# Optimization experiments

Hardware: AMD Instinct MI355X
Metric: run time of the kernel (lower is better)

The kernel has to match this reference:

```python
import jax, jax.numpy as jnp
import numpy as np

B, T, D = 1, 4096, 2048
NUM_HEADS, NUM_KV_HEADS, HEAD_DIM = 16, 8, 128
QUERY_PRE_ATTN_SCALAR = HEAD_DIM ** -0.5
SOFT_CAP = 50.0
WINDOW = 1024
ROPE_BASE = 10000.0
ROPE_SCALE = 1.0
K_MASK = -2.3819763e+38


def apply_rope(x, positions, head_dim, max_wavelength=ROPE_BASE, scale_factor=ROPE_SCALE):
    # x: [B, T, N, H], positions: [B, T]
    fraction = 2.0 * jnp.arange(head_dim // 2, dtype=jnp.float32) / head_dim
    timescale = max_wavelength ** fraction  # [H/2]
    sinusoid = positions[..., None].astype(jnp.float32) / timescale  # [B, T, H/2]
    sinusoid = (sinusoid / scale_factor)[..., None, :]  # [B, T, 1, H/2]
    sin, cos = jnp.sin(sinusoid), jnp.cos(sinusoid)
    first, second = jnp.split(x, 2, axis=-1)
    out = jnp.concatenate([first * cos - second * sin,
                           second * cos + first * sin], axis=-1)
    return out.astype(x.dtype)


def setup_inputs() -> dict:
    key = jax.random.key(0)
    ks = jax.random.split(key, 4)
    x = jax.random.normal(ks[0], (B, T, D), dtype=jnp.float32)
    segment_pos = jnp.broadcast_to(jnp.arange(T, dtype=jnp.int32), (B, T))
    # causal mask [B, T, S]
    attn_mask = jnp.broadcast_to(
        jnp.tril(jnp.ones((T, T), dtype=jnp.bool_)), (B, T, T))
    q_w = jax.random.normal(ks[1], (NUM_HEADS, D, HEAD_DIM), dtype=jnp.float32) * 0.02
    kv_w = jax.random.normal(ks[2], (2, NUM_KV_HEADS, D, HEAD_DIM), dtype=jnp.float32) * 0.02
    o_w = jax.random.normal(ks[3], (NUM_HEADS, HEAD_DIM, D), dtype=jnp.float32) * 0.02
    return {"x": x, "segment_pos": segment_pos, "attn_mask": attn_mask,
            "q_w": q_w, "kv_w": kv_w, "o_w": o_w}


def reference(x, segment_pos, attn_mask, q_w, kv_w, o_w):
    # Projections (GQA: separate q and kv einsums)
    q = jnp.einsum('BTD,NDH->BTNH', x, q_w)          # [B,T,N,H]
    k = jnp.einsum('BSD,KDH->BSKH', x, kv_w[0])      # [B,S,K,H]
    v = jnp.einsum('BSD,KDH->BSKH', x, kv_w[1])      # [B,S,K,H]

    q = apply_rope(q, segment_pos, HEAD_DIM)
    q = q * QUERY_PRE_ATTN_SCALAR
    k = apply_rope(k, segment_pos, HEAD_DIM)

    num_groups = NUM_HEADS // NUM_KV_HEADS
    qg = q.reshape(B, T, NUM_KV_HEADS, num_groups, HEAD_DIM)
    logits = jnp.einsum('BTKGH,BSKH->BTKGS', qg, k)
    logits = logits.reshape(B, T, NUM_HEADS, -1)     # [B,T,N,S]

    # soft cap
    logits = jnp.tanh(logits / SOFT_CAP) * SOFT_CAP

    # sliding-window mask combined with causal mask
    all_ones = jnp.ones_like(attn_mask)
    sliding = jnp.triu(all_ones, -WINDOW + 1) * jnp.tril(all_ones, WINDOW - 1)
    mask = sliding * attn_mask                       # [B,T,S] bool

    padded = jnp.where(mask[:, :, None, :], logits, K_MASK)
    probs = jax.nn.softmax(padded, axis=-1).astype(k.dtype)

    probs_g = probs.reshape(B, T, NUM_KV_HEADS, num_groups, -1)
    encoded = jnp.einsum('BTKGS,BSKH->BTKGH', probs_g, v)
    encoded = encoded.reshape(B, T, NUM_HEADS, HEAD_DIM)

    attn_output = jnp.einsum('BTNH,NHD->BTD', encoded, o_w)
    return attn_output
```

## Files before the change

kernel.cpp:

```cpp
#include <hip/hip_runtime.h>
#include <hip/hip_bf16.h>
#include <math.h>

typedef __attribute__((ext_vector_type(8))) short short8;
typedef __attribute__((ext_vector_type(8))) unsigned short ushort8;
typedef __attribute__((ext_vector_type(4))) float f32x4;
typedef __attribute__((ext_vector_type(2))) float f32x2;

#define T_SEQ 4096
#define D_MODEL 2048
#define N_HEADS 16
#define N_KV 8
#define HEAD_DIM 128
#define QSCALE 0.08838834764831845f

__device__ __forceinline__ float bf2f(unsigned short u) {
  union { unsigned int i; float f; } x; x.i = ((unsigned int)u) << 16; return x.f;
}
__device__ __forceinline__ unsigned short f2bf(float f) {
  union { float f; unsigned int i; } x; x.f = f;
  unsigned int i = x.i;
  unsigned int r = i + 0x7fffu + ((i >> 16) & 1u);
  return (unsigned short)(r >> 16);
}

__global__ __launch_bounds__(256) void prep_kernel(const float* __restrict__ x,
                                                   unsigned short* __restrict__ xb,
                                                   const int* __restrict__ segpos,
                                                   float2* __restrict__ tab) {
  int b = blockIdx.x;
  if (b < 4096) {
    int idx = b * 256 + threadIdx.x;
    const float4* p = reinterpret_cast<const float4*>(x) + (size_t)idx * 2;
    float4 a = p[0], c = p[1];
    ushort8 o;
    o[0] = f2bf(a.x); o[1] = f2bf(a.y); o[2] = f2bf(a.z); o[3] = f2bf(a.w);
    o[4] = f2bf(c.x); o[5] = f2bf(c.y); o[6] = f2bf(c.z); o[7] = f2bf(c.w);
    reinterpret_cast<ushort8*>(xb)[idx] = o;
  } else {
    int idx = (b - 4096) * 256 + threadIdx.x;
    int t = idx >> 6, i = idx & 63;
    float pos = (float)segpos[t];
    float ts = powf(10000.f, (float)(2 * i) / 128.f);
    float ang = pos / ts;
    tab[idx] = make_float2(sinf(ang), cosf(ang));
  }
}

__global__ __launch_bounds__(256) void wqkv_transpose_kernel(const float* __restrict__ q_w,
                                                             const float* __restrict__ kv_w,
                                                             unsigned short* __restrict__ Wt) {
  __shared__ float tile[32][33];
  int z = blockIdx.z;
  const float* src = (z < 16) ? q_w + (size_t)z * 2048 * 128
                              : kv_w + (size_t)(z - 16) * 2048 * 128;
  unsigned short* dst = Wt + (size_t)z * 128 * 2048;
  int c0 = blockIdx.x * 32, r0 = blockIdx.y * 32;
  int tx = threadIdx.x & 31, ty = threadIdx.x >> 5;
#pragma unroll
  for (int i = 0; i < 4; ++i)
    tile[ty + i * 8][tx] = src[(size_t)(r0 + ty + i * 8) * 128 + c0 + tx];
  __syncthreads();
#pragma unroll
  for (int i = 0; i < 4; ++i)
    dst[(size_t)(c0 + ty + i * 8) * 2048 + r0 + tx] = f2bf(tile[tx][ty + i * 8]);
}

__global__ __launch_bounds__(256) void ow_transpose_kernel(const float* __restrict__ src,
                                                           unsigned short* __restrict__ dst) {
  __shared__ float tile[32][33];
  int c0 = blockIdx.x * 32, r0 = blockIdx.y * 32;
  int tx = threadIdx.x & 31, ty = threadIdx.x >> 5;
#pragma unroll
  for (int i = 0; i < 4; ++i)
    tile[ty + i * 8][tx] = src[(size_t)(r0 + ty + i * 8) * 2048 + c0 + tx];
  __syncthreads();
#pragma unroll
  for (int i = 0; i < 4; ++i)
    dst[(size_t)(c0 + ty + i * 8) * 2048 + r0 + tx] = f2bf(tile[tx][ty + i * 8]);
}

#define G2L(gp, lp)                                                           \
  __builtin_amdgcn_global_load_lds(                                           \
      (const __attribute__((address_space(1))) void*)(gp),                    \
      (__attribute__((address_space(3))) void*)(lp), 16, 0, 0)
#define GBAR() asm volatile("s_barrier" ::: "memory")
#define VMW(n) asm volatile("s_waitcnt vmcnt(" #n ")" ::: "memory")
#define LG0()  asm volatile("s_waitcnt lgkmcnt(0)" ::: "memory")

template <int OUT_BF16, int MHB>
__global__ __launch_bounds__(512, 2) void gemm256_kernel(const unsigned short* __restrict__ A,
                                                         const unsigned short* __restrict__ Bt,
                                                         void* __restrict__ Cout,
                                                         int M, int N, int K) {
  extern __shared__ unsigned short smem[];
  unsigned short* ldsA = smem;
  unsigned short* ldsB = smem + 2 * MHB * 8192;
  const int tid = threadIdx.x;
  const int lane = tid & 63, wave = tid >> 6;
  const int wm = wave >> 2, wn = wave & 3;
  const int lr = lane & 15, lg = lane >> 4;
  const int swz = (lr & 7) << 3;
  const int c0s = (lg * 8) ^ swz;
  const int c1s = (32 + lg * 8) ^ swz;

  int id = blockIdx.y * gridDim.x + blockIdx.x;
  int nb = gridDim.x * gridDim.y;
  int sw = (id & 7) * (nb >> 3) + (id >> 3);
  const long brow = (long)(sw / gridDim.x) * (128 * MHB);
  const long bcol = (long)(sw % gridDim.x) * 256;

  const unsigned short* Ag = A + brow * K;
  const unsigned short* Bg = Bt + bcol * K;

  const int r0 = tid >> 3;
  const int cs = ((tid & 7) * 8) ^ ((r0 & 7) << 3);

#define ST_A(tt, b, a)                                                        \
  { G2L(Ag + (size_t)((a) * 128 + r0) * K + (size_t)(tt) * 64 + cs,           \
        ldsA + (b) * (MHB * 8192) + (a) * 8192 + tid * 8);                    \
    G2L(Ag + (size_t)((a) * 128 + r0 + 64) * K + (size_t)(tt) * 64 + cs,      \
        ldsA + (b) * (MHB * 8192) + (a) * 8192 + 4096 + tid * 8); }
#define ST_B(tt, b, h)                                                        \
  { G2L(Bg + (size_t)((h) * 128 + r0) * K + (size_t)(tt) * 64 + cs,           \
        ldsB + (b) * 16384 + (h) * 8192 + tid * 8);                           \
    G2L(Bg + (size_t)((h) * 128 + r0 + 64) * K + (size_t)(tt) * 64 + cs,      \
        ldsB + (b) * 16384 + (h) * 8192 + 4096 + tid * 8); }

  f32x4 acc[4 * MHB][4] = {};
  short8 bf[4][2];
  short8 af[4];

#define RD_B(b)                                                               \
  { const unsigned short* pb = ldsB + (b) * 16384 + wn * 4096;                \
    _Pragma("unroll")                                                         \
    for (int n = 0; n < 4; ++n) {                                             \
      bf[n][0] = *(const short8*)(pb + (n * 16 + lr) * 64 + c0s);             \
      bf[n][1] = *(const short8*)(pb + (n * 16 + lr) * 64 + c1s);             \
    } }
#define RD_A(b, mb)                                                           \
  { const unsigned short* pa = ldsA + (b) * (MHB * 8192) + wm * (MHB * 4096); \
    af[0] = *(const short8*)(pa + ((mb) * 16 + lr) * 64 + c0s);               \
    af[1] = *(const short8*)(pa + ((mb) * 16 + lr) * 64 + c1s);               \
    af[2] = *(const short8*)(pa + ((mb) * 16 + 16 + lr) * 64 + c0s);          \
    af[3] = *(const short8*)(pa + ((mb) * 16 + 16 + lr) * 64 + c1s); }
#define MFMA2(mb)                                                             \
  { __builtin_amdgcn_s_setprio(1);                                            \
    _Pragma("unroll")                                                         \
    for (int n = 0; n < 4; ++n) {                                             \
      acc[mb][n]     = __builtin_amdgcn_mfma_f32_16x16x32_bf16(af[0], bf[n][0], acc[mb][n], 0, 0, 0);     \
      acc[mb][n]     = __builtin_amdgcn_mfma_f32_16x16x32_bf16(af[1], bf[n][1], acc[mb][n], 0, 0, 0);     \
      acc[mb + 1][n] = __builtin_amdgcn_mfma_f32_16x16x32_bf16(af[2], bf[n][0], acc[mb + 1][n], 0, 0, 0); \
      acc[mb + 1][n] = __builtin_amdgcn_mfma_f32_16x16x32_bf16(af[3], bf[n][1], acc[mb + 1][n], 0, 0, 0); \
    }                                                                         \
    __builtin_amdgcn_s_setprio(0); }

  const int NT = K >> 6;

  if constexpr (MHB == 2) {
    ST_B(0, 0, 0); ST_B(0, 0, 1); ST_A(0, 0, 0); ST_A(0, 0, 1);
    ST_B(1, 1, 0); ST_B(1, 1, 1);
    VMW(4); GBAR();
    for (int j = 0; j < (NT >> 1); ++j) {
      const int c1 = 2 * j + 1, t2 = 2 * j + 2, t3 = 2 * j + 3;
      const bool s2 = t2 < NT, s3 = t3 < NT;
      RD_B(0); RD_A(0, 0); ST_A(c1, 1, 0);
      GBAR(); LG0(); MFMA2(0); GBAR();
      RD_A(0, 2); ST_A(c1, 1, 1);
      if (s2) ST_B(t2, 0, 0);
      GBAR(); LG0(); MFMA2(2); GBAR();
      RD_A(0, 4);
      if (s2) ST_B(t2, 0, 1);
      GBAR(); LG0(); MFMA2(4); GBAR();
      RD_A(0, 6);
      if (s2) { VMW(4); } else { VMW(0); }
      GBAR(); LG0(); MFMA2(6); GBAR();
      RD_B(1); RD_A(1, 0);
      if (s2) ST_A(t2, 0, 0);
      GBAR(); LG0(); MFMA2(0); GBAR();
      RD_A(1, 2);
      if (s2) ST_A(t2, 0, 1);
      if (s3) ST_B(t3, 1, 0);
      GBAR(); LG0(); MFMA2(2); GBAR();
      RD_A(1, 4);
      if (s3) ST_B(t3, 1, 1);
      GBAR(); LG0(); MFMA2(4); GBAR();
      RD_A(1, 6);
      if (s3) { VMW(4); } else { VMW(0); }
      GBAR(); LG0(); MFMA2(6); GBAR();
    }
  } else {
    ST_B(0, 0, 0); ST_B(0, 0, 1); ST_A(0, 0, 0);
    ST_B(1, 1, 0); ST_B(1, 1, 1);
    VMW(4); GBAR();
    for (int j = 0; j < (NT >> 1); ++j) {
      const int c1 = 2 * j + 1, t2 = 2 * j + 2, t3 = 2 * j + 3;
      const bool s2 = t2 < NT, s3 = t3 < NT;
      RD_B(0); RD_A(0, 0); ST_A(c1, 1, 0);
      GBAR(); LG0(); MFMA2(0); GBAR();
      RD_A(0, 2);
      if (s2) { ST_B(t2, 0, 0); ST_B(t2, 0, 1); VMW(4); } else { VMW(0); }
      GBAR(); LG0(); MFMA2(2); GBAR();
      RD_B(1); RD_A(1, 0);
      if (s2) ST_A(t2, 0, 0);
      GBAR(); LG0(); MFMA2(0); GBAR();
      RD_A(1, 2);
      if (s3) { ST_B(t3, 1, 0); ST_B(t3, 1, 1); VMW(4); } else { VMW(0); }
      GBAR(); LG0(); MFMA2(2); GBAR();
    }
  }

#undef ST_A
#undef ST_B
#undef RD_A
#undef RD_B
#undef MFMA2

#pragma unroll
  for (int m = 0; m < 4 * MHB; ++m) {
#pragma unroll
    for (int i = 0; i < 4; ++i) {
      long row = brow + wm * (64 * MHB) + m * 16 + lg * 4 + i;
#pragma unroll
      for (int n = 0; n < 4; ++n) {
        long col = bcol + wn * 64 + n * 16 + lr;
        if (OUT_BF16)
          ((unsigned short*)Cout)[row * N + col] = f2bf(acc[m][n][i]);
        else
          ((float*)Cout)[row * N + col] = acc[m][n][i];
      }
    }
  }
}

__global__ __launch_bounds__(256) void rope_vt_kernel(const unsigned short* __restrict__ raw,
                                                      const float2* __restrict__ tab,
                                                      unsigned short* __restrict__ Qb,
                                                      unsigned short* __restrict__ Kb,
                                                      unsigned short* __restrict__ Vt) {
  __shared__ unsigned short tile[32][33];
  int b = blockIdx.x;
  if (b < 3072) {
    int gid = b * 256 + threadIdx.x;
    int j = gid & 7;
    int rem = gid >> 3;
    int hs = rem % 24;
    int t = rem / 24;
    int i0 = j * 8;
    float sv[8], cv[8];
    const float2* tp = tab + t * 64 + i0;
#pragma unroll
    for (int q = 0; q < 8; ++q) { float2 sc2 = tp[q]; sv[q] = sc2.x; cv[q] = sc2.y; }
    if (hs < 16) {
      const unsigned short* p = raw + (size_t)t * 4096 + hs * 128 + i0;
      ushort8 a = *(const ushort8*)p;
      ushort8 c = *(const ushort8*)(p + 64);
      ushort8 o1, o2;
#pragma unroll
      for (int q = 0; q < 8; ++q) {
        float fa = bf2f(a[q]), fb = bf2f(c[q]);
        o1[q] = f2bf((fa * cv[q] - fb * sv[q]) * QSCALE);
        o2[q] = f2bf((fb * cv[q] + fa * sv[q]) * QSCALE);
      }
      unsigned short* qp = Qb + ((size_t)hs * T_SEQ + t) * 128 + i0;
      *(ushort8*)qp = o1;
      *(ushort8*)(qp + 64) = o2;
    } else {
      int kn = hs - 16;
      const unsigned short* p = raw + (size_t)t * 4096 + 2048 + kn * 128 + i0;
      ushort8 a = *(const ushort8*)p;
      ushort8 c = *(const ushort8*)(p + 64);
      ushort8 o1, o2;
#pragma unroll
      for (int q = 0; q < 8; ++q) {
        float fa = bf2f(a[q]), fb = bf2f(c[q]);
        o1[q] = f2bf(fa * cv[q] - fb * sv[q]);
        o2[q] = f2bf(fb * cv[q] + fa * sv[q]);
      }
      unsigned short* kp = Kb + ((size_t)kn * T_SEQ + t) * 128 + i0;
      *(ushort8*)kp = o1;
      *(ushort8*)(kp + 64) = o2;
    }
  } else {
    int id = b - 3072;
    int bx = id & 3, by = (id >> 2) & 127, bz = id >> 9;
    const unsigned short* src = raw + 3072 + (size_t)bz * 128;
    unsigned short* dst = Vt + (size_t)bz * 128 * 4096;
    int c0 = bx * 32, r0 = by * 32;
    int tx = threadIdx.x & 31, ty = threadIdx.x >> 5;
#pragma unroll
    for (int i = 0; i < 4; ++i)
      tile[ty + i * 8][tx] = src[(size_t)(r0 + ty + i * 8) * 4096 + c0 + tx];
    __syncthreads();
#pragma unroll
    for (int i = 0; i < 4; ++i)
      dst[(size_t)(c0 + ty + i * 8) * 4096 + r0 + tx] = tile[tx][ty + i * 8];
  }
}

__global__ __launch_bounds__(512, 2) void attn_kernel(const unsigned short* __restrict__ Qb,
                                                      const unsigned short* __restrict__ Kb,
                                                      const unsigned short* __restrict__ Vt,
                                                      unsigned short* __restrict__ enc) {
  __shared__ unsigned short Ks[2][64][128];
  __shared__ unsigned short Vs[2][128][64];
  __shared__ unsigned short Ps[8][32][72];
  int rawb = blockIdx.x;
  int lin = (rawb & 7) * 32 + (rawb >> 3);
  const int h = lin >> 4;
  const int qb0 = (lin & 15) * 256;
  const int kvh = h >> 1;
  const int tid = threadIdx.x, lane = tid & 63, wave = tid >> 6;
  const int qw = qb0 + wave * 32;
  const int lr = lane & 15, lg = lane >> 4;
  const int sw = (lr & 7) << 3;
  const int ck0 = (lg * 8) ^ sw, ck1 = (32 + lg * 8) ^ sw;
  const int ck2 = (64 + lg * 8) ^ sw, ck3 = (96 + lg * 8) ^ sw;

  short8 aq[2][4];
#pragma unroll
  for (int g = 0; g < 2; ++g) {
    const unsigned short* qp = Qb + ((size_t)h * T_SEQ + qw + g * 16 + lr) * 128 + lg * 8;
#pragma unroll
    for (int c = 0; c < 4; ++c) aq[g][c] = *(const short8*)(qp + c * 32);
  }
  f32x4 acc[2][8] = {};
  float lsum[2] = {0.f, 0.f};

  const int s_lo = (qb0 - 1023) > 0 ? (qb0 - 1023) : 0;
  const int kb_lo = s_lo >> 6, kb_hi = (qb0 + 255) >> 6;

  const int rK = tid >> 4;
  const int cpK = (tid & 15) * 8;
  const int colK = cpK ^ ((rK & 7) << 3);
  const int rV = tid >> 3;
  const int cpV = (tid & 7) * 8;
  const int colV = cpV ^ ((rV & 7) << 3);
  const unsigned short* kgb = Kb + ((size_t)kvh * T_SEQ + rK) * 128 + colK;
  const unsigned short* vgb = Vt + ((size_t)kvh * 128 + rV) * T_SEQ + colV;

  ushort8 kr0, kr1, vr0, vr1;
  {
    const int s0g = kb_lo * 64;
    kr0 = *(const ushort8*)(kgb + (size_t)s0g * 128);
    kr1 = *(const ushort8*)(kgb + (size_t)(s0g + 32) * 128);
    vr0 = *(const ushort8*)(vgb + s0g);
    vr1 = *(const ushort8*)(vgb + (size_t)64 * T_SEQ + s0g);
  }

  const int qg0 = qw + lr, qg1 = qw + 16 + lr;
  for (int kb = kb_lo; kb <= kb_hi; ++kb) {
    const int s0g = kb * 64;
    const int buf = kb & 1;
    *(ushort8*)&Ks[buf][rK][cpK] = kr0;
    *(ushort8*)&Ks[buf][rK + 32][cpK] = kr1;
    *(ushort8*)&Vs[buf][rV][cpV] = vr0;
    *(ushort8*)&Vs[buf][rV + 64][cpV] = vr1;
    __syncthreads();
    if (kb < kb_hi) {
      const int sn = s0g + 64;
      kr0 = *(const ushort8*)(kgb + (size_t)sn * 128);
      kr1 = *(const ushort8*)(kgb + (size_t)(sn + 32) * 128);
      vr0 = *(const ushort8*)(vgb + sn);
      vr1 = *(const ushort8*)(vgb + (size_t)64 * T_SEQ + sn);
    }
    if (s0g > qw + 31 || s0g + 63 < qw - 1023) continue;
    const bool interior = (s0g + 63 <= qw) && (s0g >= qw - 992);

    f32x4 sT0[4] = {}, sT1[4] = {};
    __builtin_amdgcn_s_setprio(1);
#pragma unroll
    for (int st = 0; st < 4; ++st) {
      const unsigned short* kp = &Ks[buf][st * 16 + lr][0];
      short8 k0 = *(const short8*)(kp + ck0);
      short8 k1 = *(const short8*)(kp + ck1);
      short8 k2 = *(const short8*)(kp + ck2);
      short8 k3 = *(const short8*)(kp + ck3);
      sT0[st] = __builtin_amdgcn_mfma_f32_16x16x32_bf16(k0, aq[0][0], sT0[st], 0, 0, 0);
      sT1[st] = __builtin_amdgcn_mfma_f32_16x16x32_bf16(k0, aq[1][0], sT1[st], 0, 0, 0);
      sT0[st] = __builtin_amdgcn_mfma_f32_16x16x32_bf16(k1, aq[0][1], sT0[st], 0, 0, 0);
      sT1[st] = __builtin_amdgcn_mfma_f32_16x16x32_bf16(k1, aq[1][1], sT1[st], 0, 0, 0);
      sT0[st] = __builtin_amdgcn_mfma_f32_16x16x32_bf16(k2, aq[0][2], sT0[st], 0, 0, 0);
      sT1[st] = __builtin_amdgcn_mfma_f32_16x16x32_bf16(k2, aq[1][2], sT1[st], 0, 0, 0);
      sT0[st] = __builtin_amdgcn_mfma_f32_16x16x32_bf16(k3, aq[0][3], sT0[st], 0, 0, 0);
      sT1[st] = __builtin_amdgcn_mfma_f32_16x16x32_bf16(k3, aq[1][3], sT1[st], 0, 0, 0);
    }
    __builtin_amdgcn_s_setprio(0);

#pragma unroll
    for (int g = 0; g < 2; ++g) {
      const f32x4* sTg = g ? sT1 : sT0;
      const int qgg = g ? qg1 : qg0;
#pragma unroll
      for (int st = 0; st < 4; ++st) {
        f32x4 svv = sTg[st];
        f32x2 sa, sb;
        sa[0] = svv[0]; sa[1] = svv[1]; sb[0] = svv[2]; sb[1] = svv[3];
        f32x2 ua = sa * sa, ub = sb * sb;
        f32x2 numa = ua * 4.0e-4f + 15.f, numb = ub * 4.0e-4f + 15.f;
        f32x2 dena = ua * 2.4e-3f + 15.f, denb = ub * 2.4e-3f + 15.f;
        f32x2 ra, rb;
        ra[0] = __builtin_amdgcn_rcpf(dena[0]); ra[1] = __builtin_amdgcn_rcpf(dena[1]);
        rb[0] = __builtin_amdgcn_rcpf(denb[0]); rb[1] = __builtin_amdgcn_rcpf(denb[1]);
        f32x2 ea = (sa * 1.44269504f) * numa * ra;
        f32x2 eb = (sb * 1.44269504f) * numb * rb;
        float e[4] = {ea[0], ea[1], eb[0], eb[1]};
        float p[4];
#pragma unroll
        for (int r = 0; r < 4; ++r) {
          if (!interior) {
            int sg = s0g + st * 16 + lg * 4 + r;
            e[r] = ((unsigned)(qgg - sg) <= 1023u) ? e[r] : -__builtin_inff();
          }
          asm("v_exp_f32 %0, %1" : "=v"(p[r]) : "v"(e[r]));
        }
        lsum[g] += (p[0] + p[1]) + (p[2] + p[3]);
        unsigned u0, u1;
        asm("v_cvt_pk_bf16_f32 %0, %1, %2" : "=v"(u0) : "v"(p[0]), "v"(p[1]));
        asm("v_cvt_pk_bf16_f32 %0, %1, %2" : "=v"(u1) : "v"(p[2]), "v"(p[3]));
        uint2 w; w.x = u0; w.y = u1;
        *(uint2*)&Ps[wave][g * 16 + lr][st * 16 + lg * 4] = w;
      }
    }
    short8 pa00 = *(const short8*)&Ps[wave][lr][lg * 8];
    short8 pa01 = *(const short8*)&Ps[wave][lr][32 + lg * 8];
    short8 pa10 = *(const short8*)&Ps[wave][16 + lr][lg * 8];
    short8 pa11 = *(const short8*)&Ps[wave][16 + lr][32 + lg * 8];
    __builtin_amdgcn_s_setprio(1);
#pragma unroll
    for (int d0 = 0; d0 < 8; ++d0) {
      const unsigned short* vp = &Vs[buf][d0 * 16 + lr][0];
      short8 bv0 = *(const short8*)(vp + ((lg * 8) ^ sw));
      short8 bv1 = *(const short8*)(vp + ((32 + lg * 8) ^ sw));
      acc[0][d0] = __builtin_amdgcn_mfma_f32_16x16x32_bf16(pa00, bv0, acc[0][d0], 0, 0, 0);
      acc[1][d0] = __builtin_amdgcn_mfma_f32_16x16x32_bf16(pa10, bv0, acc[1][d0], 0, 0, 0);
      acc[0][d0] = __builtin_amdgcn_mfma_f32_16x16x32_bf16(pa01, bv1, acc[0][d0], 0, 0, 0);
      acc[1][d0] = __builtin_amdgcn_mfma_f32_16x16x32_bf16(pa11, bv1, acc[1][d0], 0, 0, 0);
    }
    __builtin_amdgcn_s_setprio(0);
  }

#pragma unroll
  for (int g = 0; g < 2; ++g) {
    float l = lsum[g];
    l += __shfl_xor(l, 16);
    l += __shfl_xor(l, 32);
#pragma unroll
    for (int r = 0; r < 4; ++r) {
      float lt = __shfl(l, lg * 4 + r);
      float inv = __builtin_amdgcn_rcpf(lt);
      int row = qw + g * 16 + lg * 4 + r;
      unsigned short* op = enc + (size_t)row * D_MODEL + h * 128 + lr;
#pragma unroll
      for (int d0 = 0; d0 < 8; ++d0) op[d0 * 16] = f2bf(acc[g][d0][r] * inv);
    }
  }
}

extern "C" void kernel_launch(void* const* d_in, const int* in_sizes, int n_in,
                              void* d_out, int out_size, void* d_ws, size_t ws_size,
                              hipStream_t stream) {
  const float* x = (const float*)d_in[0];
  const int* segpos = (const int*)d_in[1];
  const float* q_w = (const float*)d_in[3];
  const float* kv_w = (const float*)d_in[4];
  const float* o_w = (const float*)d_in[5];
  float* out = (float*)d_out;
  char* ws = (char*)d_ws;

  const size_t OFF_XB = 0;
  const size_t OFF_WT = OFF_XB + 16777216;
  const size_t OFF_RAW = OFF_WT + 16777216;
  const size_t OFF_KB = OFF_RAW + 33554432;
  const size_t OFF_VT = OFF_KB + 8388608;
  const size_t OFF_TAB = OFF_VT + 8388608;
  unsigned short* xb = (unsigned short*)(ws + OFF_XB);
  unsigned short* Wt = (unsigned short*)(ws + OFF_WT);
  unsigned short* raw = (unsigned short*)(ws + OFF_RAW);
  unsigned short* Kb = (unsigned short*)(ws + OFF_KB);
  unsigned short* Vt = (unsigned short*)(ws + OFF_VT);
  float2* tab = (float2*)(ws + OFF_TAB);
  unsigned short* o_wt = xb;
  unsigned short* Qb = Wt;
  unsigned short* enc = raw;

  hipFuncSetAttribute((const void*)(gemm256_kernel<1, 2>),
                      hipFuncAttributeMaxDynamicSharedMemorySize, 131072);
  hipFuncSetAttribute((const void*)(gemm256_kernel<0, 1>),
                      hipFuncAttributeMaxDynamicSharedMemorySize, 98304);

  prep_kernel<<<dim3(5120), dim3(256), 0, stream>>>(x, xb, segpos, tab);
  wqkv_transpose_kernel<<<dim3(4, 64, 32), dim3(256), 0, stream>>>(q_w, kv_w, Wt);
  gemm256_kernel<1, 2><<<dim3(16, 16), dim3(512), 131072, stream>>>(xb, Wt, (void*)raw, 4096, 4096, 2048);
  ow_transpose_kernel<<<dim3(64, 64), dim3(256), 0, stream>>>(o_w, o_wt);
  rope_vt_kernel<<<dim3(7168), dim3(256), 0, stream>>>(raw, tab, Qb, Kb, Vt);
  attn_kernel<<<dim3(256), dim3(512), 0, stream>>>(Qb, Kb, Vt, enc);
  gemm256_kernel<0, 1><<<dim3(8, 32), dim3(512), 98304, stream>>>(enc, o_wt, (void*)out, 4096, 2048, 2048);
}
```

Baseline: 197.4 us.

## Use triple-buffered LDS pipeline for the output-projection GEMM

Adds a dedicated GEMM kernel for the output projection (128x256 tiles) that uses a three-stage LDS ring buffer, prefetching two K-tiles ahead instead of one. The QKV GEMM template drops its MHB parameter and keeps only the 256x256 path. The aim is to hide more global-load latency in the out-projection GEMM. In exchange it uses 144 KB of LDS per block, limiting occupancy to one block per CU.

```diff
diff --git a/kernel.cpp b/kernel.cpp
--- a/kernel.cpp
+++ b/kernel.cpp
@@ -88,14 +88,14 @@
 #define VMW(n) asm volatile("s_waitcnt vmcnt(" #n ")" ::: "memory")
 #define LG0()  asm volatile("s_waitcnt lgkmcnt(0)" ::: "memory")
 
-template <int OUT_BF16, int MHB>
+template <int OUT_BF16>
 __global__ __launch_bounds__(512, 2) void gemm256_kernel(const unsigned short* __restrict__ A,
                                                          const unsigned short* __restrict__ Bt,
                                                          void* __restrict__ Cout,
                                                          int M, int N, int K) {
   extern __shared__ unsigned short smem[];
   unsigned short* ldsA = smem;
-  unsigned short* ldsB = smem + 2 * MHB * 8192;
+  unsigned short* ldsB = smem + 32768;
   const int tid = threadIdx.x;
   const int lane = tid & 63, wave = tid >> 6;
   const int wm = wave >> 2, wn = wave & 3;
@@ -107,7 +107,7 @@
   int id = blockIdx.y * gridDim.x + blockIdx.x;
   int nb = gridDim.x * gridDim.y;
   int sw = (id & 7) * (nb >> 3) + (id >> 3);
-  const long brow = (long)(sw / gridDim.x) * (128 * MHB);
+  const long brow = (long)(sw / gridDim.x) * 256;
   const long bcol = (long)(sw % gridDim.x) * 256;
 
   const unsigned short* Ag = A + brow * K;
@@ -118,16 +118,16 @@
 
 #define ST_A(tt, b, a)                                                        \
   { G2L(Ag + (size_t)((a) * 128 + r0) * K + (size_t)(tt) * 64 + cs,           \
-        ldsA + (b) * (MHB * 8192) + (a) * 8192 + tid * 8);                    \
+        ldsA + (b) * 16384 + (a) * 8192 + tid * 8);                           \
     G2L(Ag + (size_t)((a) * 128 + r0 + 64) * K + (size_t)(tt) * 64 + cs,      \
-        ldsA + (b) * (MHB * 8192) + (a) * 8192 + 4096 + tid * 8); }
+        ldsA + (b) * 16384 + (a) * 8192 + 4096 + tid * 8); }
 #define ST_B(tt, b, h)                                                        \
   { G2L(Bg + (size_t)((h) * 128 + r0) * K + (size_t)(tt) * 64 + cs,           \
         ldsB + (b) * 16384 + (h) * 8192 + tid * 8);                           \
     G2L(Bg + (size_t)((h) * 128 + r0 + 64) * K + (size_t)(tt) * 64 + cs,      \
         ldsB + (b) * 16384 + (h) * 8192 + 4096 + tid * 8); }
 
-  f32x4 acc[4 * MHB][4] = {};
+  f32x4 acc[8][4] = {};
   short8 bf[4][2];
   short8 af[4];
 
@@ -139,7 +139,7 @@
       bf[n][1] = *(const short8*)(pb + (n * 16 + lr) * 64 + c1s);             \
     } }
 #define RD_A(b, mb)                                                           \
-  { const unsigned short* pa = ldsA + (b) * (MHB * 8192) + wm * (MHB * 4096); \
+  { const unsigned short* pa = ldsA + (b) * 16384 + wm * 8192;                \
     af[0] = *(const short8*)(pa + ((mb) * 16 + lr) * 64 + c0s);               \
     af[1] = *(const short8*)(pa + ((mb) * 16 + lr) * 64 + c1s);               \
     af[2] = *(const short8*)(pa + ((mb) * 16 + 16 + lr) * 64 + c0s);          \
@@ -156,71 +156,43 @@
     __builtin_amdgcn_s_setprio(0); }
 
   const int NT = K >> 6;
-
-  if constexpr (MHB == 2) {
-    ST_B(0, 0, 0); ST_B(0, 0, 1); ST_A(0, 0, 0); ST_A(0, 0, 1);
-    ST_B(1, 1, 0); ST_B(1, 1, 1);
-    VMW(4); GBAR();
-    for (int j = 0; j < (NT >> 1); ++j) {
-      const int c1 = 2 * j + 1, t2 = 2 * j + 2, t3 = 2 * j + 3;
-      const bool s2 = t2 < NT, s3 = t3 < NT;
-      RD_B(0); RD_A(0, 0); ST_A(c1, 1, 0);
-      GBAR(); LG0(); MFMA2(0); GBAR();
-      RD_A(0, 2); ST_A(c1, 1, 1);
-      if (s2) ST_B(t2, 0, 0);
-      GBAR(); LG0(); MFMA2(2); GBAR();
-      RD_A(0, 4);
-      if (s2) ST_B(t2, 0, 1);
-      GBAR(); LG0(); MFMA2(4); GBAR();
-      RD_A(0, 6);
-      if (s2) { VMW(4); } else { VMW(0); }
-      GBAR(); LG0(); MFMA2(6); GBAR();
-      RD_B(1); RD_A(1, 0);
-      if (s2) ST_A(t2, 0, 0);
-      GBAR(); LG0(); MFMA2(0); GBAR();
-      RD_A(1, 2);
-      if (s2) ST_A(t2, 0, 1);
-      if (s3) ST_B(t3, 1, 0);
-      GBAR(); LG0(); MFMA2(2); GBAR();
-      RD_A(1, 4);
-      if (s3) ST_B(t3, 1, 1);
-      GBAR(); LG0(); MFMA2(4); GBAR();
-      RD_A(1, 6);
-      if (s3) { VMW(4); } else { VMW(0); }
-      GBAR(); LG0(); MFMA2(6); GBAR();
-    }
-  } else {
-    ST_B(0, 0, 0); ST_B(0, 0, 1); ST_A(0, 0, 0);
-    ST_B(1, 1, 0); ST_B(1, 1, 1);
-    VMW(4); GBAR();
-    for (int j = 0; j < (NT >> 1); ++j) {
-      const int c1 = 2 * j + 1, t2 = 2 * j + 2, t3 = 2 * j + 3;
-      const bool s2 = t2 < NT, s3 = t3 < NT;
-      RD_B(0); RD_A(0, 0); ST_A(c1, 1, 0);
-      GBAR(); LG0(); MFMA2(0); GBAR();
-      RD_A(0, 2);
-      if (s2) { ST_B(t2, 0, 0); ST_B(t2, 0, 1); VMW(4); } else { VMW(0); }
-      GBAR(); LG0(); MFMA2(2); GBAR();
-      RD_B(1); RD_A(1, 0);
-      if (s2) ST_A(t2, 0, 0);
-      GBAR(); LG0(); MFMA2(0); GBAR();
-      RD_A(1, 2);
-      if (s3) { ST_B(t3, 1, 0); ST_B(t3, 1, 1); VMW(4); } else { VMW(0); }
-      GBAR(); LG0(); MFMA2(2); GBAR();
-    }
-  }
-
-#undef ST_A
-#undef ST_B
-#undef RD_A
-#undef RD_B
-#undef MFMA2
-
-#pragma unroll
-  for (int m = 0; m < 4 * MHB; ++m) {
+  ST_B(0, 0, 0); ST_B(0, 0, 1); ST_A(0, 0, 0); ST_A(0, 0, 1);
+  ST_B(1, 1, 0); ST_B(1, 1, 1);
+  VMW(4); GBAR();
+  for (int j = 0; j < (NT >> 1); ++j) {
+    const int c1 = 2 * j + 1, t2 = 2 * j + 2, t3 = 2 * j + 3;
+    const bool s2 = t2 < NT, s3 = t3 < NT;
+    RD_B(0); RD_A(0, 0); ST_A(c1, 1, 0);
+    GBAR(); LG0(); MFMA2(0); GBAR();
+    RD_A(0, 2); ST_A(c1, 1, 1);
+    if (s2) ST_B(t2, 0, 0);
+    GBAR(); LG0(); MFMA2(2); GBAR();
+    RD_A(0, 4);
+    if (s2) ST_B(t2, 0, 1);
+    GBAR(); LG0(); MFMA2(4); GBAR();
+    RD_A(0, 6);
+    if (s2) { VMW(4); } else { VMW(0); }
+    GBAR(); LG0(); MFMA2(6); GBAR();
+    RD_B(1); RD_A(1, 0);
+    if (s2) ST_A(t2, 0, 0);
+    GBAR(); LG0(); MFMA2(0); GBAR();
+    RD_A(1, 2);
+    if (s2) ST_A(t2, 0, 1);
+    if (s3) ST_B(t3, 1, 0);
+    GBAR(); LG0(); MFMA2(2); GBAR();
+    RD_A(1, 4);
+    if (s3) ST_B(t3, 1, 1);
+    GBAR(); LG0(); MFMA2(4); GBAR();
+    RD_A(1, 6);
+    if (s3) { VMW(4); } else { VMW(0); }
+    GBAR(); LG0(); MFMA2(6); GBAR();
+  }
+
+#pragma unroll
+  for (int m = 0; m < 8; ++m) {
 #pragma unroll
     for (int i = 0; i < 4; ++i) {
-      long row = brow + wm * (64 * MHB) + m * 16 + lg * 4 + i;
+      long row = brow + wm * 128 + m * 16 + lg * 4 + i;
 #pragma unroll
       for (int n = 0; n < 4; ++n) {
         long col = bcol + wn * 64 + n * 16 + lr;
@@ -231,6 +203,113 @@
       }
     }
   }
+#undef ST_A
+#undef ST_B
+#undef RD_A
+#undef RD_B
+#undef MFMA2
+}
+
+__global__ __launch_bounds__(512, 1) void gemm_op3_kernel(const unsigned short* __restrict__ A,
+                                                          const unsigned short* __restrict__ Bt,
+                                                          float* __restrict__ Cout,
+                                                          int M, int N, int K) {
+  extern __shared__ unsigned short smem[];
+  unsigned short* ldsA = smem;
+  unsigned short* ldsB = smem + 3 * 8192;
+  const int tid = threadIdx.x;
+  const int lane = tid & 63, wave = tid >> 6;
+  const int wm = wave >> 2, wn = wave & 3;
+  const int lr = lane & 15, lg = lane >> 4;
+  const int swz = (lr & 7) << 3;
+  const int c0s = (lg * 8) ^ swz;
+  const int c1s = (32 + lg * 8) ^ swz;
+
+  int id = blockIdx.y * gridDim.x + blockIdx.x;
+  int nb = gridDim.x * gridDim.y;
+  int sw = (id & 7) * (nb >> 3) + (id >> 3);
+  const long brow = (long)(sw / gridDim.x) * 128;
+  const long bcol = (long)(sw % gridDim.x) * 256;
+
+  const unsigned short* Ag = A + brow * K;
+  const unsigned short* Bg = Bt + bcol * K;
+
+  const int r0 = tid >> 3;
+  const int cs = ((tid & 7) * 8) ^ ((r0 & 7) << 3);
+
+#define ST_A3(tt, b)                                                          \
+  { G2L(Ag + (size_t)(r0) * K + (size_t)(tt) * 64 + cs,                       \
+        ldsA + (b) * 8192 + tid * 8);                                         \
+    G2L(Ag + (size_t)(r0 + 64) * K + (size_t)(tt) * 64 + cs,                  \
+        ldsA + (b) * 8192 + 4096 + tid * 8); }
+#define ST_B3(tt, b, h)                                                       \
+  { G2L(Bg + (size_t)((h) * 128 + r0) * K + (size_t)(tt) * 64 + cs,           \
+        ldsB + (b) * 16384 + (h) * 8192 + tid * 8);                           \
+    G2L(Bg + (size_t)((h) * 128 + r0 + 64) * K + (size_t)(tt) * 64 + cs,      \
+        ldsB + (b) * 16384 + (h) * 8192 + 4096 + tid * 8); }
+
+  f32x4 acc[4][4] = {};
+  short8 bf[4][2];
+  short8 af[4];
+
+#define RD_B3(b)                                                              \
+  { const unsigned short* pb = ldsB + (b) * 16384 + wn * 4096;                \
+    _Pragma("unroll")                                                         \
+    for (int n = 0; n < 4; ++n) {                                             \
+      bf[n][0] = *(const short8*)(pb + (n * 16 + lr) * 64 + c0s);             \
+      bf[n][1] = *(const short8*)(pb + (n * 16 + lr) * 64 + c1s);             \
+    } }
+#define RD_A3(b, mb)                                                          \
+  { const unsigned short* pa = ldsA + (b) * 8192 + wm * 4096;                 \
+    af[0] = *(const short8*)(pa + ((mb) * 16 + lr) * 64 + c0s);               \
+    af[1] = *(const short8*)(pa + ((mb) * 16 + lr) * 64 + c1s);               \
+    af[2] = *(const short8*)(pa + ((mb) * 16 + 16 + lr) * 64 + c0s);          \
+    af[3] = *(const short8*)(pa + ((mb) * 16 + 16 + lr) * 64 + c1s); }
+#define MFMA2(mb)                                                             \
+  { __builtin_amdgcn_s_setprio(1);                                            \
+    _Pragma("unroll")                                                         \
+    for (int n = 0; n < 4; ++n) {                                             \
+      acc[mb][n]     = __builtin_amdgcn_mfma_f32_16x16x32_bf16(af[0], bf[n][0], acc[mb][n], 0, 0, 0);     \
+      acc[mb][n]     = __builtin_amdgcn_mfma_f32_16x16x32_bf16(af[1], bf[n][1], acc[mb][n], 0, 0, 0);     \
+      acc[mb + 1][n] = __builtin_amdgcn_mfma_f32_16x16x32_bf16(af[2], bf[n][0], acc[mb + 1][n], 0, 0, 0); \
+      acc[mb + 1][n] = __builtin_amdgcn_mfma_f32_16x16x32_bf16(af[3], bf[n][1], acc[mb + 1][n], 0, 0, 0); \
+    }                                                                         \
+    __builtin_amdgcn_s_setprio(0); }
+
+  const int NT = K >> 6;
+  ST_B3(0, 0, 0); ST_B3(0, 0, 1); ST_A3(0, 0);
+  ST_B3(1, 1, 0); ST_B3(1, 1, 1); ST_A3(1, 1);
+  VMW(6); GBAR();
+  int b = 0;
+  for (int t = 0; t < NT; ++t) {
+    int bn = b + 2; if (bn >= 3) bn -= 3;
+    const bool st = (t + 2) < NT;
+    RD_B3(b); RD_A3(b, 0);
+    if (st) { ST_B3(t + 2, bn, 0); ST_B3(t + 2, bn, 1); }
+    GBAR(); LG0(); MFMA2(0); GBAR();
+    RD_A3(b, 2);
+    if (st) { ST_A3(t + 2, bn); VMW(6); } else { VMW(0); }
+    GBAR(); LG0(); MFMA2(2); GBAR();
+    b = b + 1; if (b >= 3) b = 0;
+  }
+
+#pragma unroll
+  for (int m = 0; m < 4; ++m) {
+#pragma unroll
+    for (int i = 0; i < 4; ++i) {
+      long row = brow + wm * 64 + m * 16 + lg * 4 + i;
+#pragma unroll
+      for (int n = 0; n < 4; ++n) {
+        long col = bcol + wn * 64 + n * 16 + lr;
+        Cout[row * N + col] = acc[m][n][i];
+      }
+    }
+  }
+#undef ST_A3
+#undef ST_B3
+#undef RD_A3
+#undef RD_B3
+#undef MFMA2
 }
 
 __global__ __launch_bounds__(256) void rope_vt_kernel(const unsigned short* __restrict__ raw,
@@ -484,16 +563,16 @@
   unsigned short* Qb = Wt;
   unsigned short* enc = raw;
 
-  hipFuncSetAttribute((const void*)(gemm256_kernel<1, 2>),
+  hipFuncSetAttribute((const void*)(gemm256_kernel<1>),
                       hipFuncAttributeMaxDynamicSharedMemorySize, 131072);
-  hipFuncSetAttribute((const void*)(gemm256_kernel<0, 1>),
-                      hipFuncAttributeMaxDynamicSharedMemorySize, 98304);
+  hipFuncSetAttribute((const void*)gemm_op3_kernel,
+                      hipFuncAttributeMaxDynamicSharedMemorySize, 147456);
 
   prep_kernel<<<dim3(5120), dim3(256), 0, stream>>>(x, xb, segpos, tab);
   wqkv_transpose_kernel<<<dim3(4, 64, 32), dim3(256), 0, stream>>>(q_w, kv_w, Wt);
-  gemm256_kernel<1, 2><<<dim3(16, 16), dim3(512), 131072, stream>>>(xb, Wt, (void*)raw, 4096, 4096, 2048);
+  gemm256_kernel<1><<<dim3(16, 16), dim3(512), 131072, stream>>>(xb, Wt, (void*)raw, 4096, 4096, 2048);
   ow_transpose_kernel<<<dim3(64, 64), dim3(256), 0, stream>>>(o_w, o_wt);
   rope_vt_kernel<<<dim3(7168), dim3(256), 0, stream>>>(raw, tab, Qb, Kb, Vt);
   attn_kernel<<<dim3(256), dim3(512), 0, stream>>>(Qb, Kb, Vt, enc);
-  gemm256_kernel<0, 1><<<dim3(8, 32), dim3(512), 98304, stream>>>(enc, o_wt, (void*)out, 4096, 2048, 2048);
-}
+  gemm_op3_kernel<<<dim3(8, 32), dim3(512), 147456, stream>>>(enc, o_wt, out, 4096, 2048, 2048);
+}
```

Measured after the change: 199.1 us. Within noise of the previous version (+0.9%).

## Split-K output projection with atomics and fuse o_w transpose into rope kernel

Applied to the files above, without the earlier changes.

The output-projection GEMM now uses 256x256 tiles with a split-K of 2 over the grid z dimension, accumulating into a zeroed fp32 output with atomic adds. The o_w transpose is folded into the rope/V-transpose kernel as extra blocks, which removes one launch. The GEMM template is unified around the 2-row-half schedule. The extra cost is a memset of the output and atomic traffic to global memory, and the float summation order becomes nondeterministic.

```diff
diff --git a/kernel.cpp b/kernel.cpp
--- a/kernel.cpp
+++ b/kernel.cpp
@@ -66,20 +66,6 @@
     dst[(size_t)(c0 + ty + i * 8) * 2048 + r0 + tx] = f2bf(tile[tx][ty + i * 8]);
 }
 
-__global__ __launch_bounds__(256) void ow_transpose_kernel(const float* __restrict__ src,
-                                                           unsigned short* __restrict__ dst) {
-  __shared__ float tile[32][33];
-  int c0 = blockIdx.x * 32, r0 = blockIdx.y * 32;
-  int tx = threadIdx.x & 31, ty = threadIdx.x >> 5;
-#pragma unroll
-  for (int i = 0; i < 4; ++i)
-    tile[ty + i * 8][tx] = src[(size_t)(r0 + ty + i * 8) * 2048 + c0 + tx];
-  __syncthreads();
-#pragma unroll
-  for (int i = 0; i < 4; ++i)
-    dst[(size_t)(c0 + ty + i * 8) * 2048 + r0 + tx] = f2bf(tile[tx][ty + i * 8]);
-}
-
 #define G2L(gp, lp)                                                           \
   __builtin_amdgcn_global_load_lds(                                           \
       (const __attribute__((address_space(1))) void*)(gp),                    \
@@ -88,14 +74,14 @@
 #define VMW(n) asm volatile("s_waitcnt vmcnt(" #n ")" ::: "memory")
 #define LG0()  asm volatile("s_waitcnt lgkmcnt(0)" ::: "memory")
 
-template <int OUT_BF16, int MHB>
+template <int OUT_MODE>
 __global__ __launch_bounds__(512, 2) void gemm256_kernel(const unsigned short* __restrict__ A,
                                                          const unsigned short* __restrict__ Bt,
                                                          void* __restrict__ Cout,
                                                          int M, int N, int K) {
   extern __shared__ unsigned short smem[];
   unsigned short* ldsA = smem;
-  unsigned short* ldsB = smem + 2 * MHB * 8192;
+  unsigned short* ldsB = smem + 32768;
   const int tid = threadIdx.x;
   const int lane = tid & 63, wave = tid >> 6;
   const int wm = wave >> 2, wn = wave & 3;
@@ -107,27 +93,30 @@
   int id = blockIdx.y * gridDim.x + blockIdx.x;
   int nb = gridDim.x * gridDim.y;
   int sw = (id & 7) * (nb >> 3) + (id >> 3);
-  const long brow = (long)(sw / gridDim.x) * (128 * MHB);
+  const long brow = (long)(sw / gridDim.x) * 256;
   const long bcol = (long)(sw % gridDim.x) * 256;
-
-  const unsigned short* Ag = A + brow * K;
-  const unsigned short* Bg = Bt + bcol * K;
+  long koff = 0;
+  int klen = K;
+  if constexpr (OUT_MODE == 2) { klen = K >> 1; koff = (long)blockIdx.z * klen; }
+
+  const unsigned short* Ag = A + brow * K + koff;
+  const unsigned short* Bg = Bt + bcol * K + koff;
 
   const int r0 = tid >> 3;
   const int cs = ((tid & 7) * 8) ^ ((r0 & 7) << 3);
 
 #define ST_A(tt, b, a)                                                        \
   { G2L(Ag + (size_t)((a) * 128 + r0) * K + (size_t)(tt) * 64 + cs,           \
-        ldsA + (b) * (MHB * 8192) + (a) * 8192 + tid * 8);                    \
+        ldsA + (b) * 16384 + (a) * 8192 + tid * 8);                           \
     G2L(Ag + (size_t)((a) * 128 + r0 + 64) * K + (size_t)(tt) * 64 + cs,      \
-        ldsA + (b) * (MHB * 8192) + (a) * 8192 + 4096 + tid * 8); }
+        ldsA + (b) * 16384 + (a) * 8192 + 4096 + tid * 8); }
 #define ST_B(tt, b, h)                                                        \
   { G2L(Bg + (size_t)((h) * 128 + r0) * K + (size_t)(tt) * 64 + cs,           \
         ldsB + (b) * 16384 + (h) * 8192 + tid * 8);                           \
     G2L(Bg + (size_t)((h) * 128 + r0 + 64) * K + (size_t)(tt) * 64 + cs,      \
         ldsB + (b) * 16384 + (h) * 8192 + 4096 + tid * 8); }
 
-  f32x4 acc[4 * MHB][4] = {};
+  f32x4 acc[8][4] = {};
   short8 bf[4][2];
   short8 af[4];
 
@@ -139,7 +128,7 @@
       bf[n][1] = *(const short8*)(pb + (n * 16 + lr) * 64 + c1s);             \
     } }
 #define RD_A(b, mb)                                                           \
-  { const unsigned short* pa = ldsA + (b) * (MHB * 8192) + wm * (MHB * 4096); \
+  { const unsigned short* pa = ldsA + (b) * 16384 + wm * 8192;                \
     af[0] = *(const short8*)(pa + ((mb) * 16 + lr) * 64 + c0s);               \
     af[1] = *(const short8*)(pa + ((mb) * 16 + lr) * 64 + c1s);               \
     af[2] = *(const short8*)(pa + ((mb) * 16 + 16 + lr) * 64 + c0s);          \
@@ -155,90 +144,70 @@
     }                                                                         \
     __builtin_amdgcn_s_setprio(0); }
 
-  const int NT = K >> 6;
-
-  if constexpr (MHB == 2) {
-    ST_B(0, 0, 0); ST_B(0, 0, 1); ST_A(0, 0, 0); ST_A(0, 0, 1);
-    ST_B(1, 1, 0); ST_B(1, 1, 1);
-    VMW(4); GBAR();
-    for (int j = 0; j < (NT >> 1); ++j) {
-      const int c1 = 2 * j + 1, t2 = 2 * j + 2, t3 = 2 * j + 3;
-      const bool s2 = t2 < NT, s3 = t3 < NT;
-      RD_B(0); RD_A(0, 0); ST_A(c1, 1, 0);
-      GBAR(); LG0(); MFMA2(0); GBAR();
-      RD_A(0, 2); ST_A(c1, 1, 1);
-      if (s2) ST_B(t2, 0, 0);
-      GBAR(); LG0(); MFMA2(2); GBAR();
-      RD_A(0, 4);
-      if (s2) ST_B(t2, 0, 1);
-      GBAR(); LG0(); MFMA2(4); GBAR();
-      RD_A(0, 6);
-      if (s2) { VMW(4); } else { VMW(0); }
-      GBAR(); LG0(); MFMA2(6); GBAR();
-      RD_B(1); RD_A(1, 0);
-      if (s2) ST_A(t2, 0, 0);
-      GBAR(); LG0(); MFMA2(0); GBAR();
-      RD_A(1, 2);
-      if (s2) ST_A(t2, 0, 1);
-      if (s3) ST_B(t3, 1, 0);
-      GBAR(); LG0(); MFMA2(2); GBAR();
-      RD_A(1, 4);
-      if (s3) ST_B(t3, 1, 1);
-      GBAR(); LG0(); MFMA2(4); GBAR();
-      RD_A(1, 6);
-      if (s3) { VMW(4); } else { VMW(0); }
-      GBAR(); LG0(); MFMA2(6); GBAR();
-    }
-  } else {
-    ST_B(0, 0, 0); ST_B(0, 0, 1); ST_A(0, 0, 0);
-    ST_B(1, 1, 0); ST_B(1, 1, 1);
-    VMW(4); GBAR();
-    for (int j = 0; j < (NT >> 1); ++j) {
-      const int c1 = 2 * j + 1, t2 = 2 * j + 2, t3 = 2 * j + 3;
-      const bool s2 = t2 < NT, s3 = t3 < NT;
-      RD_B(0); RD_A(0, 0); ST_A(c1, 1, 0);
-      GBAR(); LG0(); MFMA2(0); GBAR();
-      RD_A(0, 2);
-      if (s2) { ST_B(t2, 0, 0); ST_B(t2, 0, 1); VMW(4); } else { VMW(0); }
-      GBAR(); LG0(); MFMA2(2); GBAR();
-      RD_B(1); RD_A(1, 0);
-      if (s2) ST_A(t2, 0, 0);
-      GBAR(); LG0(); MFMA2(0); GBAR();
-      RD_A(1, 2);
-      if (s3) { ST_B(t3, 1, 0); ST_B(t3, 1, 1); VMW(4); } else { VMW(0); }
-      GBAR(); LG0(); MFMA2(2); GBAR();
-    }
-  }
-
+  const int NT = klen >> 6;
+  ST_B(0, 0, 0); ST_B(0, 0, 1); ST_A(0, 0, 0); ST_A(0, 0, 1);
+  ST_B(1, 1, 0); ST_B(1, 1, 1);
+  VMW(4); GBAR();
+  for (int j = 0; j < (NT >> 1); ++j) {
+    const int c1 = 2 * j + 1, t2 = 2 * j + 2, t3 = 2 * j + 3;
+    const bool s2 = t2 < NT, s3 = t3 < NT;
+    RD_B(0); RD_A(0, 0); ST_A(c1, 1, 0);
+    GBAR(); LG0(); MFMA2(0); GBAR();
+    RD_A(0, 2); ST_A(c1, 1, 1);
+    if (s2) ST_B(t2, 0, 0);
+    GBAR(); LG0(); MFMA2(2); GBAR();
+    RD_A(0, 4);
+    if (s2) ST_B(t2, 0, 1);
+    GBAR(); LG0(); MFMA2(4); GBAR();
+    RD_A(0, 6);
+    if (s2) { VMW(4); } else { VMW(0); }
+    GBAR(); LG0(); MFMA2(6); GBAR();
+    RD_B(1); RD_A(1, 0);
+    if (s2) ST_A(t2, 0, 0);
+    GBAR(); LG0(); MFMA2(0); GBAR();
+    RD_A(1, 2);
+    if (s2) ST_A(t2, 0, 1);
+    if (s3) ST_B(t3, 1, 0);
+    GBAR(); LG0(); MFMA2(2); GBAR();
+    RD_A(1, 4);
+    if (s3) ST_B(t3, 1, 1);
+    GBAR(); LG0(); MFMA2(4); GBAR();
+    RD_A(1, 6);
+    if (s3) { VMW(4); } else { VMW(0); }
+    GBAR(); LG0(); MFMA2(6); GBAR();
+  }
+
+#pragma unroll
+  for (int m = 0; m < 8; ++m) {
+#pragma unroll
+    for (int i = 0; i < 4; ++i) {
+      long row = brow + wm * 128 + m * 16 + lg * 4 + i;
+#pragma unroll
+      for (int n = 0; n < 4; ++n) {
+        long col = bcol + wn * 64 + n * 16 + lr;
+        if constexpr (OUT_MODE == 1)
+          ((unsigned short*)Cout)[row * N + col] = f2bf(acc[m][n][i]);
+        else
+          unsafeAtomicAdd(&((float*)Cout)[row * N + col], acc[m][n][i]);
+      }
+    }
+  }
 #undef ST_A
 #undef ST_B
 #undef RD_A
 #undef RD_B
 #undef MFMA2
-
-#pragma unroll
-  for (int m = 0; m < 4 * MHB; ++m) {
-#pragma unroll
-    for (int i = 0; i < 4; ++i) {
-      long row = brow + wm * (64 * MHB) + m * 16 + lg * 4 + i;
-#pragma unroll
-      for (int n = 0; n < 4; ++n) {
-        long col = bcol + wn * 64 + n * 16 + lr;
-        if (OUT_BF16)
-          ((unsigned short*)Cout)[row * N + col] = f2bf(acc[m][n][i]);
-        else
-          ((float*)Cout)[row * N + col] = acc[m][n][i];
-      }
-    }
-  }
-}
-
-__global__ __launch_bounds__(256) void rope_vt_kernel(const unsigned short* __restrict__ raw,
-                                                      const float2* __restrict__ tab,
-                                                      unsigned short* __restrict__ Qb,
-                                                      unsigned short* __restrict__ Kb,
-                                                      unsigned short* __restrict__ Vt) {
-  __shared__ unsigned short tile[32][33];
+}
+
+__global__ __launch_bounds__(256) void rope_vt_ow_kernel(const unsigned short* __restrict__ raw,
+                                                         const float2* __restrict__ tab,
+                                                         unsigned short* __restrict__ Qb,
+                                                         unsigned short* __restrict__ Kb,
+                                                         unsigned short* __restrict__ Vt,
+                                                         const float* __restrict__ o_w,
+                                                         unsigned short* __restrict__ o_wt) {
+  __shared__ unsigned short tileU[32][33];
+  __shared__ float tileF[32][33];
   int b = blockIdx.x;
   if (b < 3072) {
     int gid = b * 256 + threadIdx.x;
@@ -281,7 +250,7 @@
       *(ushort8*)kp = o1;
       *(ushort8*)(kp + 64) = o2;
     }
-  } else {
+  } else if (b < 7168) {
     int id = b - 3072;
     int bx = id & 3, by = (id >> 2) & 127, bz = id >> 9;
     const unsigned short* src = raw + 3072 + (size_t)bz * 128;
@@ -290,11 +259,23 @@
     int tx = threadIdx.x & 31, ty = threadIdx.x >> 5;
 #pragma unroll
     for (int i = 0; i < 4; ++i)
-      tile[ty + i * 8][tx] = src[(size_t)(r0 + ty + i * 8) * 4096 + c0 + tx];
+      tileU[ty + i * 8][tx] = src[(size_t)(r0 + ty + i * 8) * 4096 + c0 + tx];
     __syncthreads();
 #pragma unroll
     for (int i = 0; i < 4; ++i)
-      dst[(size_t)(c0 + ty + i * 8) * 4096 + r0 + tx] = tile[tx][ty + i * 8];
+      dst[(size_t)(c0 + ty + i * 8) * 4096 + r0 + tx] = tileU[tx][ty + i * 8];
+  } else {
+    int id = b - 7168;
+    int bx = id & 63, by = id >> 6;
+    int c0 = bx * 32, r0 = by * 32;
+    int tx = threadIdx.x & 31, ty = threadIdx.x >> 5;
+#pragma unroll
+    for (int i = 0; i < 4; ++i)
+      tileF[ty + i * 8][tx] = o_w[(size_t)(r0 + ty + i * 8) * 2048 + c0 + tx];
+    __syncthreads();
+#pragma unroll
+    for (int i = 0; i < 4; ++i)
+      o_wt[(size_t)(c0 + ty + i * 8) * 2048 + r0 + tx] = f2bf(tileF[tx][ty + i * 8]);
   }
 }
 
@@ -484,16 +465,16 @@
   unsigned short* Qb = Wt;
   unsigned short* enc = raw;
 
-  hipFuncSetAttribute((const void*)(gemm256_kernel<1, 2>),
+  hipFuncSetAttribute((const void*)(gemm256_kernel<1>),
                       hipFuncAttributeMaxDynamicSharedMemorySize, 131072);
-  hipFuncSetAttribute((const void*)(gemm256_kernel<0, 1>),
-                      hipFuncAttributeMaxDynamicSharedMemorySize, 98304);
-
+  hipFuncSetAttribute((const void*)(gemm256_kernel<2>),
+                      hipFuncAttributeMaxDynamicSharedMemorySize, 131072);
+
+  hipMemsetAsync(out, 0, (size_t)out_size * sizeof(float), stream);
   prep_kernel<<<dim3(5120), dim3(256), 0, stream>>>(x, xb, segpos, tab);
   wqkv_transpose_kernel<<<dim3(4, 64, 32), dim3(256), 0, stream>>>(q_w, kv_w, Wt);
-  gemm256_kernel<1, 2><<<dim3(16, 16), dim3(512), 131072, stream>>>(xb, Wt, (void*)raw, 4096, 4096, 2048);
-  ow_transpose_kernel<<<dim3(64, 64), dim3(256), 0, stream>>>(o_w, o_wt);
-  rope_vt_kernel<<<dim3(7168), dim3(256), 0, stream>>>(raw, tab, Qb, Kb, Vt);
+  gemm256_kernel<1><<<dim3(16, 16), dim3(512), 131072, stream>>>(xb, Wt, (void*)raw, 4096, 4096, 2048);
+  rope_vt_ow_kernel<<<dim3(11264), dim3(256), 0, stream>>>(raw, tab, Qb, Kb, Vt, o_w, o_wt);
   attn_kernel<<<dim3(256), dim3(512), 0, stream>>>(Qb, Kb, Vt, enc);
-  gemm256_kernel<0, 1><<<dim3(8, 32), dim3(512), 98304, stream>>>(enc, o_wt, (void*)out, 4096, 2048, 2048);
-}
+  gemm256_kernel<2><<<dim3(8, 16, 2), dim3(512), 131072, stream>>>(enc, o_wt, (void*)out, 4096, 2048, 2048);
+}
```

Measured after the change: 244.7 us. 1.24x slower.
